# Kernel optimization log

Measured on AMD Instinct MI355X. Metric: run time of the kernel, lower is better.

## Reference

```python
import jax, jax.numpy as jnp
import numpy as np
import math

NUM_HEADS = 32
HEAD_SIZE = 128
NUM_KV_HEADS = 8
GROUP = NUM_HEADS // NUM_KV_HEADS  # num_queries_per_kv
NEG_FILL = -50000.0


def setup_inputs() -> dict:
    key = jax.random.key(0)
    k1, k2, k3 = jax.random.split(key, 3)
    B, S = 2, 2048
    query = jax.random.normal(k1, (B, S, NUM_HEADS * HEAD_SIZE), dtype=jnp.float32)
    kk = jax.random.normal(k2, (B, S, NUM_KV_HEADS * HEAD_SIZE), dtype=jnp.float32)
    vv = jax.random.normal(k3, (B, S, NUM_KV_HEADS * HEAD_SIZE), dtype=jnp.float32)
    return {"query": query, "key": kk, "value": vv}


def _gqa_attention(query, key, value):
    B, S, H = query.shape
    # [B, nh, S, d]
    q = query.reshape(B, S, NUM_HEADS, HEAD_SIZE).transpose(0, 2, 1, 3)
    # expand kv heads to nh via group broadcast (matches expand+reshape in torch)
    k = key.reshape(B, S, NUM_KV_HEADS, HEAD_SIZE)
    k = jnp.broadcast_to(k[:, :, :, None, :], (B, S, NUM_KV_HEADS, GROUP, HEAD_SIZE))
    k = k.reshape(B, S, NUM_HEADS, HEAD_SIZE).transpose(0, 2, 1, 3)
    v = value.reshape(B, S, NUM_KV_HEADS, HEAD_SIZE)
    v = jnp.broadcast_to(v[:, :, :, None, :], (B, S, NUM_KV_HEADS, GROUP, HEAD_SIZE))
    v = v.reshape(B, S, NUM_HEADS, HEAD_SIZE).transpose(0, 2, 1, 3)

    scale = 1.0 / math.sqrt(HEAD_SIZE)  # code uses sqrt(d_k), not self.scale
    scores = jnp.einsum('bhqd,bhkd->bhqk', q, k) * scale  # [B, nh, S, S]
    causal = jnp.tril(jnp.ones((S, S), dtype=bool))  # subsequent_mask
    scores = jnp.where(causal[None, None, :, :], scores, NEG_FILL)
    p_attn = jax.nn.softmax(scores, axis=-1)
    out = jnp.einsum('bhqk,bhkd->bhqd', p_attn, v)  # [B, nh, S, d]
    return out.transpose(0, 2, 1, 3).reshape(B, S, H)


def reference(query, key, value):
    return _gqa_attention(query, key, value)
```

## Files before the change

kernel.cpp:

```cpp
#include <hip/hip_runtime.h>
#include <hip/hip_bf16.h>


namespace {
constexpr int NH = 32;
constexpr int HD = 128;
constexpr int KVH = 8;
constexpr int SEQ = 2048;
constexpr int NB = 2;
constexpr int QSTRIDE = NH * HD;
constexpr int KSTRIDE = KVH * HD;
constexpr float SCALE = 0.08838834764831845f;
constexpr float SCALE2 = 0.12751744f;

typedef __attribute__((ext_vector_type(8))) short short8;
typedef __attribute__((ext_vector_type(8))) __bf16 bf16x8;
typedef __attribute__((ext_vector_type(4))) float f32x4;
typedef __attribute__((ext_vector_type(16))) float f32x16;
typedef __attribute__((ext_vector_type(2))) unsigned uint2v;
typedef __attribute__((ext_vector_type(4))) unsigned uint4v;

__device__ inline short cvt_bf16(float f) {
  unsigned u = __builtin_bit_cast(unsigned, f);
  unsigned r = (u + 0x7fffu + ((u >> 16) & 1u)) >> 16;
  return (short)r;
}

__device__ inline short8 cvt8(const float* p) {
  f32x4 a = *(const f32x4*)p;
  f32x4 b = *(const f32x4*)(p + 4);
  short8 r;
#pragma unroll
  for (int j = 0; j < 4; ++j) {
    r[j] = cvt_bf16(a[j]);
    r[j + 4] = cvt_bf16(b[j]);
  }
  return r;
}

__device__ inline short8 cvt8s(const float* p, float sc) {
  f32x4 a = *(const f32x4*)p;
  f32x4 b = *(const f32x4*)(p + 4);
  short8 r;
#pragma unroll
  for (int j = 0; j < 4; ++j) {
    r[j] = cvt_bf16(a[j] * sc);
    r[j + 4] = cvt_bf16(b[j] * sc);
  }
  return r;
}

__device__ inline bf16x8 asbf(short8 s) { return __builtin_bit_cast(bf16x8, s); }

__device__ inline unsigned cvt_pk_bf16(float lo, float hi) {
  unsigned r;
  asm("v_cvt_pk_bf16_f32 %0, %1, %2" : "=v"(r) : "v"(lo), "v"(hi));
  return r;
}

__device__ inline float fast_exp2(float x) {
#if __has_builtin(__builtin_amdgcn_exp2f)
  return __builtin_amdgcn_exp2f(x);
#else
  return __expf(x * 0.6931471805599453f);
#endif
}

__device__ inline void swap_halves(unsigned a, unsigned b, unsigned& lo,
                                   unsigned& hi, int half) {
#if __has_builtin(__builtin_amdgcn_permlane32_swap)
  (void)half;
  uint2v r = __builtin_amdgcn_permlane32_swap(a, b, false, false);
  lo = r[0];
  hi = r[1];
#else
  unsigned axf = (unsigned)__shfl_xor((int)a, 32);
  unsigned bxf = (unsigned)__shfl_xor((int)b, 32);
  lo = half ? bxf : a;
  hi = half ? b : axf;
#endif
}
}

__global__ __launch_bounds__(256) void convert_kv(const float* __restrict__ K,
                                                  const float* __restrict__ V,
                                                  short* __restrict__ Kbf,
                                                  short* __restrict__ Vtb) {
  __shared__ __align__(16) short t_sh[32 * 136];
  int bid = blockIdx.x;
  int tid = threadIdx.x;
  if (bid < 2048) {
    int flat = bid * 256 + tid;
    int c16 = flat & 15;
    int kvh = (flat >> 4) & 7;
    int s = (flat >> 7) & 2047;
    int b = flat >> 18;
    int dsrc = (c16 ^ (s & 7)) << 3;
    const float* src = K + ((size_t)(b * SEQ + s)) * KSTRIDE + kvh * HD + dsrc;
    short* dst = Kbf + ((size_t)(b * KVH + kvh) * SEQ + s) * HD + (c16 << 3);
    *(short8*)dst = cvt8(src);
    return;
  }
  bid -= 2048;
  int s0 = (bid & 63) * 32;
  int kvh = (bid >> 6) & 7;
  int b = bid >> 9;
  {
    int si = tid >> 3;
    int dseg = (tid & 7) * 16;
    const float* src = V + ((size_t)(b * SEQ + s0 + si)) * KSTRIDE + kvh * HD + dseg;
    short8 a0 = cvt8(src);
    short8 a1 = cvt8(src + 8);
    *(short8*)&t_sh[si * 136 + dseg] = a0;
    *(short8*)&t_sh[si * 136 + dseg + 8] = a1;
  }
  __syncthreads();
  {
    int d = tid >> 1;
    int sseg = (tid & 1) * 16;
    short8 o0, o1;
#pragma unroll
    for (int j = 0; j < 8; ++j) {
      o0[j] = t_sh[(sseg + j) * 136 + d];
      o1[j] = t_sh[(sseg + 8 + j) * 136 + d];
    }
    int m7 = d & 7;
    int cs0 = ((s0 & 63) >> 3) + (sseg >> 3);
    short* dstv = Vtb + (size_t)(b * KVH + kvh) * HD * SEQ +
                  (size_t)(s0 >> 6) * (HD * 64) + d * 64;
    *(short8*)(dstv + ((cs0 ^ m7) << 3)) = o0;
    *(short8*)(dstv + (((cs0 + 1) ^ m7) << 3)) = o1;
  }
}

__global__ __launch_bounds__(256, 2) void gqa_attn(
    const float* __restrict__ Q, const short* __restrict__ Kbf,
    const short* __restrict__ Vtb, float* __restrict__ O) {
  __shared__ __align__(16) short k_sh[2][64 * 128];
  __shared__ __align__(16) short v_sh[2][128 * 64];

  const int tid = threadIdx.x;
  const int wid = tid >> 6;
  const int lane = tid & 63;
  const int l31 = lane & 31;
  const int half = lane >> 5;
  const int vx = (((l31 & 7) ^ half) << 4);

  const int bid = blockIdx.x;
  const int qt = 15 - (bid >> 6);
  const int h = bid & 31;
  const int b = (bid >> 5) & 1;
  const int kvh = h >> 2;
  const int q0 = qt << 7;

  const int row_min = q0 + wid * 32;
  const int row_top = row_min + 31;
  const int qrow = row_min + l31;

  const float* qptr = Q + (size_t)(b * SEQ + qrow) * QSTRIDE + h * HD + half * 8;
  short8 qf[8];
#pragma unroll
  for (int st = 0; st < 8; ++st) qf[st] = cvt8s(qptr + st * 16, SCALE2);

  f32x16 acc[4];
#pragma unroll
  for (int t = 0; t < 4; ++t)
#pragma unroll
    for (int i = 0; i < 16; ++i) acc[t][i] = 0.f;
  float l_acc[2] = {0.f, 0.f};

  const char* kbase = (const char*)(Kbf + (size_t)(b * KVH + kvh) * SEQ * HD);
  const char* vbase = (const char*)(Vtb + (size_t)(b * KVH + kvh) * HD * SEQ);
  const int sgo = wid * 4096 + lane * 16;

  auto stage = [&](int bsel, int kb_) {
    const char* kg = kbase + (size_t)kb_ * 256 + sgo;
    const char* vg = vbase + (size_t)(kb_ >> 6) * 16384 + sgo;
    char* kl = (char*)&k_sh[bsel][0] + wid * 4096;
    char* vl = (char*)&v_sh[bsel][0] + wid * 4096;
#pragma unroll
    for (int i = 0; i < 4; ++i) {
      __builtin_amdgcn_global_load_lds((const void*)(kg + i * 1024),
                                       (void*)(kl + i * 1024), 16, 0, 0);
      __builtin_amdgcn_global_load_lds((const void*)(vg + i * 1024),
                                       (void*)(vl + i * 1024), 16, 0, 0);
    }
  };

  const int nT = 2 * qt + 2;
  stage(0, 0);

#pragma unroll 1
  for (int it = 0; it < nT; ++it) {
    const int kb = it << 6;
    const int cur = it & 1;
    __syncthreads();
    if (it + 1 < nT) stage(cur ^ 1, kb + 64);

    if (kb <= row_top) {
      const char* kB = (const char*)&k_sh[cur][0] + l31 * 256;
      const char* vB = (const char*)&v_sh[cur][0] + l31 * 128;

      f32x16 cS[2];
#pragma unroll
      for (int s = 0; s < 2; ++s)
#pragma unroll
        for (int i = 0; i < 16; ++i) cS[s][i] = 0.f;
#pragma unroll
      for (int st = 0; st < 8; ++st) {
        const int so = vx ^ (st << 5);
        bf16x8 qv = asbf(qf[st]);
        short8 k0 = *(const short8*)(kB + so);
        cS[0] = __builtin_amdgcn_mfma_f32_32x32x16_bf16(asbf(k0), qv, cS[0], 0, 0, 0);
        short8 k1 = *(const short8*)(kB + 8192 + so);
        cS[1] = __builtin_amdgcn_mfma_f32_32x32x16_bf16(asbf(k1), qv, cS[1], 0, 0, 0);
      }

      const bool diag = (kb + 63 > row_min);
      const int rel = qrow - kb - 4 * half;
#pragma unroll
      for (int s = 0; s < 2; ++s) {
        if (diag) {
#pragma unroll
          for (int r = 0; r < 16; ++r) {
            const int kc_ = (r & 3) + 8 * (r >> 2);
            float sc = cS[s][r];
            if (kc_ + s * 32 > rel) sc = -1e30f;
            float e = fast_exp2(sc);
            cS[s][r] = e;
            l_acc[s] += e;
          }
        } else {
#pragma unroll
          for (int r = 0; r < 16; ++r) {
            float e = fast_exp2(cS[s][r]);
            cS[s][r] = e;
            l_acc[s] += e;
          }
        }

        unsigned Ag[4], Bg[4];
#pragma unroll
        for (int g = 0; g < 4; ++g) {
          Ag[g] = cvt_pk_bf16(cS[s][4 * g], cS[s][4 * g + 1]);
          Bg[g] = cvt_pk_bf16(cS[s][4 * g + 2], cS[s][4 * g + 3]);
        }
#pragma unroll
        for (int kc = 0; kc < 2; ++kc) {
          unsigned a_lo, a_hi, b_lo, b_hi;
          swap_halves(Ag[2 * kc], Ag[2 * kc + 1], a_lo, a_hi, half);
          swap_halves(Bg[2 * kc], Bg[2 * kc + 1], b_lo, b_hi, half);
          uint4v wv;
          wv[0] = a_lo;
          wv[1] = b_lo;
          wv[2] = a_hi;
          wv[3] = b_hi;
          bf16x8 pa = __builtin_bit_cast(bf16x8, wv);
          const int vo = vx ^ ((s << 6) | (kc << 5));
#pragma unroll
          for (int t = 0; t < 4; ++t) {
            short8 vv = *(const short8*)(vB + t * 4096 + vo);
            acc[t] = __builtin_amdgcn_mfma_f32_32x32x16_bf16(pa, asbf(vv), acc[t], 0, 0, 0);
          }
        }
      }
    }
  }

  float l_part = l_acc[0] + l_acc[1];
  float lsum = l_part + __shfl_xor(l_part, 32);
  float invv = 1.f / lsum;
  float inv_i[16];
#pragma unroll
  for (int i = 0; i < 16; ++i)
    inv_i[i] = __shfl(invv, (i & 3) + 8 * (i >> 2) + 4 * half);
  float* ob = O + (size_t)(b * SEQ + row_min) * QSTRIDE + h * HD;
#pragma unroll
  for (int t = 0; t < 4; ++t)
#pragma unroll
    for (int i = 0; i < 16; ++i) {
      const int row = (i & 3) + 8 * (i >> 2) + 4 * half;
      ob[(size_t)row * QSTRIDE + t * 32 + l31] = acc[t][i] * inv_i[i];
    }
}

namespace {
constexpr int FKL = 136, FVL = 40, FPL = 40;
constexpr float NEGF = -50000.0f;
}
__global__ __launch_bounds__(256) void gqa_attn_f32(
    const float* __restrict__ Q, const float* __restrict__ K,
    const float* __restrict__ V, float* __restrict__ O) {
  __shared__ __align__(16) short k_sh[32 * FKL];
  __shared__ __align__(16) short v_sh[HD * FVL];
  __shared__ __align__(16) short p_sh[4 * 16 * FPL];
  const int tid = threadIdx.x, wid = tid >> 6, lane = tid & 63;
  const int col = lane & 15, quad = lane >> 4;
  const int bid = blockIdx.x;
  const int qt = bid & 31, h = (bid >> 5) & 31, b = bid >> 10;
  const int kvh = h >> 2, q0 = qt << 6;
  const int qrow = q0 + wid * 16 + col;
  const float* qptr = Q + (size_t)(b * SEQ + qrow) * QSTRIDE + h * HD + quad * 8;
  short8 qf[4];
#pragma unroll
  for (int c = 0; c < 4; ++c) qf[c] = cvt8(qptr + c * 32);
  f32x4 acc[8];
#pragma unroll
  for (int t = 0; t < 8; ++t) acc[t] = (f32x4){0.f, 0.f, 0.f, 0.f};
  float m_run[4] = {-1e30f, -1e30f, -1e30f, -1e30f};
  float l_run[4] = {0.f, 0.f, 0.f, 0.f};
  const float* kbase = K + (size_t)b * SEQ * KSTRIDE + kvh * HD;
  const float* vbase = V + (size_t)b * SEQ * KSTRIDE + kvh * HD;
  const int skey = tid & 31, sd = (tid >> 5) << 4;
  const int q_reg_row = q0 + wid * 16 + quad * 4;
  const int nT = (q0 >> 5) + 2;
  for (int it = 0; it < nT; ++it) {
    const int kb = it << 5;
    __syncthreads();
    {
      const float* ks = kbase + (size_t)(kb + skey) * KSTRIDE + sd;
      short8 k0 = cvt8(ks), k1 = cvt8(ks + 8);
      *(short8*)&k_sh[skey * FKL + sd] = k0;
      *(short8*)&k_sh[skey * FKL + sd + 8] = k1;
      const float* vs = vbase + (size_t)(kb + skey) * KSTRIDE + sd;
      short8 v0 = cvt8(vs), v1 = cvt8(vs + 8);
#pragma unroll
      for (int j = 0; j < 8; ++j) v_sh[(sd + j) * FVL + skey] = v0[j];
#pragma unroll
      for (int j = 0; j < 8; ++j) v_sh[(sd + 8 + j) * FVL + skey] = v1[j];
    }
    __syncthreads();
    f32x4 cL = {0.f, 0.f, 0.f, 0.f}, cR = {0.f, 0.f, 0.f, 0.f};
#pragma unroll
    for (int c = 0; c < 4; ++c) {
      short8 bL = *(const short8*)&k_sh[col * FKL + c * 32 + quad * 8];
      short8 bR = *(const short8*)&k_sh[(col + 16) * FKL + c * 32 + quad * 8];
      cL = __builtin_amdgcn_mfma_f32_16x16x32_bf16(asbf(qf[c]), asbf(bL), cL, 0, 0, 0);
      cR = __builtin_amdgcn_mfma_f32_16x16x32_bf16(asbf(qf[c]), asbf(bR), cR, 0, 0, 0);
    }
    float pL[4], pR[4], alpha[4];
#pragma unroll
    for (int r = 0; r < 4; ++r) {
      const int qr = q_reg_row + r;
      float sL = (kb + col <= qr) ? cL[r] * SCALE : NEGF;
      float sR = (kb + 16 + col <= qr) ? cR[r] * SCALE : NEGF;
      float mx = fmaxf(sL, sR);
      mx = fmaxf(mx, __shfl_xor(mx, 1));
      mx = fmaxf(mx, __shfl_xor(mx, 2));
      mx = fmaxf(mx, __shfl_xor(mx, 4));
      mx = fmaxf(mx, __shfl_xor(mx, 8));
      float nm = fmaxf(m_run[r], mx);
      alpha[r] = __expf(m_run[r] - nm);
      m_run[r] = nm;
      pL[r] = __expf(sL - nm);
      pR[r] = __expf(sR - nm);
      float ps = pL[r] + pR[r];
      ps += __shfl_xor(ps, 1);
      ps += __shfl_xor(ps, 2);
      ps += __shfl_xor(ps, 4);
      ps += __shfl_xor(ps, 8);
      l_run[r] = l_run[r] * alpha[r] + ps;
    }
#pragma unroll
    for (int t = 0; t < 8; ++t)
#pragma unroll
      for (int r = 0; r < 4; ++r) acc[t][r] *= alpha[r];
    short* pw = &p_sh[wid * 16 * FPL];
#pragma unroll
    for (int r = 0; r < 4; ++r) {
      pw[(quad * 4 + r) * FPL + col] = cvt_bf16(pL[r]);
      pw[(quad * 4 + r) * FPL + col + 16] = cvt_bf16(pR[r]);
    }
    __syncthreads();
    short8 pa = *(const short8*)&pw[col * FPL + quad * 8];
#pragma unroll
    for (int t = 0; t < 8; ++t) {
      short8 vb = *(const short8*)&v_sh[(t * 16 + col) * FVL + quad * 8];
      acc[t] = __builtin_amdgcn_mfma_f32_16x16x32_bf16(asbf(pa), asbf(vb), acc[t], 0, 0, 0);
    }
  }
  float inv[4];
#pragma unroll
  for (int r = 0; r < 4; ++r) inv[r] = 1.f / l_run[r];
  float* ob = O + (size_t)(b * SEQ + q_reg_row) * QSTRIDE + h * HD;
#pragma unroll
  for (int r = 0; r < 4; ++r)
#pragma unroll
    for (int t = 0; t < 8; ++t)
      ob[(size_t)r * QSTRIDE + t * 16 + col] = acc[t][r] * inv[r];
}

extern "C" void kernel_launch(void* const* d_in, const int* in_sizes, int n_in,
                              void* d_out, int out_size, void* d_ws, size_t ws_size,
                              hipStream_t stream) {
  const float* Q = (const float*)d_in[0];
  const float* K = (const float*)d_in[1];
  const float* V = (const float*)d_in[2];
  float* O = (float*)d_out;
  const size_t kv_elems = (size_t)NB * KVH * SEQ * HD;
  const size_t need = kv_elems * 2 * sizeof(short);
  if (ws_size >= need) {
    short* Kbf = (short*)d_ws;
    short* Vtb = Kbf + kv_elems;
    convert_kv<<<3072, 256, 0, stream>>>(K, V, Kbf, Vtb);
    gqa_attn<<<1024, 256, 0, stream>>>(Q, Kbf, Vtb, O);
  } else {
    gqa_attn_f32<<<2048, 256, 0, stream>>>(Q, K, V, O);
  }
}
```

Measured before the change: 208.9 us.

## Process two query heads per block to reuse staged K/V tiles

Each block now handles two query heads that share the same KV head, so every K/V tile staged into LDS and every K/V register fragment feeds two sets of MFMAs. The grid is halved to 512 blocks, and the query-tile order interleaves long and short causal tiles to balance the load. This halves LDS staging and K/V LDS reads per unit of work. In exchange it doubles the accumulator and Q-fragment register footprint, which may hurt occupancy under launch_bounds(256,2), and fewer blocks means less parallelism.

```diff
diff --git a/kernel.cpp b/kernel.cpp
--- a/kernel.cpp
+++ b/kernel.cpp
@@ -147,27 +147,32 @@
   const int vx = (((l31 & 7) ^ half) << 4);
 
   const int bid = blockIdx.x;
-  const int qt = 15 - (bid >> 6);
-  const int h = bid & 31;
-  const int b = (bid >> 5) & 1;
-  const int kvh = h >> 2;
+  const int g = bid >> 5;
+  const int qt = (bid < 256) ? (15 - g) : (g - 8);
+  const int idx = bid & 31;
+  const int hp = idx & 15;
+  const int b = idx >> 4;
+  const int h0 = hp * 2;
+  const int kvh = hp >> 1;
   const int q0 = qt << 7;
 
   const int row_min = q0 + wid * 32;
   const int row_top = row_min + 31;
   const int qrow = row_min + l31;
 
-  const float* qptr = Q + (size_t)(b * SEQ + qrow) * QSTRIDE + h * HD + half * 8;
-  short8 qf[8];
-#pragma unroll
-  for (int st = 0; st < 8; ++st) qf[st] = cvt8s(qptr + st * 16, SCALE2);
-
-  f32x16 acc[4];
+  const float* qp = Q + (size_t)(b * SEQ + qrow) * QSTRIDE + h0 * HD + half * 8;
+  short8 qa[8], qb[8];
+#pragma unroll
+  for (int st = 0; st < 8; ++st) qa[st] = cvt8s(qp + st * 16, SCALE2);
+#pragma unroll
+  for (int st = 0; st < 8; ++st) qb[st] = cvt8s(qp + HD + st * 16, SCALE2);
+
+  f32x16 acc0[4], acc1[4];
 #pragma unroll
   for (int t = 0; t < 4; ++t)
 #pragma unroll
-    for (int i = 0; i < 16; ++i) acc[t][i] = 0.f;
-  float l_acc[2] = {0.f, 0.f};
+    for (int i = 0; i < 16; ++i) { acc0[t][i] = 0.f; acc1[t][i] = 0.f; }
+  float la0 = 0.f, la1 = 0.f;
 
   const char* kbase = (const char*)(Kbf + (size_t)(b * KVH + kvh) * SEQ * HD);
   const char* vbase = (const char*)(Vtb + (size_t)(b * KVH + kvh) * HD * SEQ);
@@ -201,87 +206,109 @@
       const char* kB = (const char*)&k_sh[cur][0] + l31 * 256;
       const char* vB = (const char*)&v_sh[cur][0] + l31 * 128;
 
-      f32x16 cS[2];
-#pragma unroll
-      for (int s = 0; s < 2; ++s)
-#pragma unroll
-        for (int i = 0; i < 16; ++i) cS[s][i] = 0.f;
-#pragma unroll
-      for (int st = 0; st < 8; ++st) {
-        const int so = vx ^ (st << 5);
-        bf16x8 qv = asbf(qf[st]);
-        short8 k0 = *(const short8*)(kB + so);
-        cS[0] = __builtin_amdgcn_mfma_f32_32x32x16_bf16(asbf(k0), qv, cS[0], 0, 0, 0);
-        short8 k1 = *(const short8*)(kB + 8192 + so);
-        cS[1] = __builtin_amdgcn_mfma_f32_32x32x16_bf16(asbf(k1), qv, cS[1], 0, 0, 0);
-      }
-
       const bool diag = (kb + 63 > row_min);
       const int rel = qrow - kb - 4 * half;
+
 #pragma unroll
       for (int s = 0; s < 2; ++s) {
+        f32x16 c0, c1;
+#pragma unroll
+        for (int i = 0; i < 16; ++i) { c0[i] = 0.f; c1[i] = 0.f; }
+#pragma unroll
+        for (int st = 0; st < 8; ++st) {
+          const int so = vx ^ (st << 5);
+          short8 k0 = *(const short8*)(kB + s * 8192 + so);
+          bf16x8 kb16 = asbf(k0);
+          c0 = __builtin_amdgcn_mfma_f32_32x32x16_bf16(kb16, asbf(qa[st]), c0, 0, 0, 0);
+          c1 = __builtin_amdgcn_mfma_f32_32x32x16_bf16(kb16, asbf(qb[st]), c1, 0, 0, 0);
+        }
+
         if (diag) {
 #pragma unroll
           for (int r = 0; r < 16; ++r) {
-            const int kc_ = (r & 3) + 8 * (r >> 2);
-            float sc = cS[s][r];
-            if (kc_ + s * 32 > rel) sc = -1e30f;
-            float e = fast_exp2(sc);
-            cS[s][r] = e;
-            l_acc[s] += e;
+            const int kc_ = (r & 3) + 8 * (r >> 2) + s * 32;
+            const bool msk = kc_ > rel;
+            float s0v = msk ? -1e30f : c0[r];
+            float s1v = msk ? -1e30f : c1[r];
+            float e0 = fast_exp2(s0v);
+            float e1 = fast_exp2(s1v);
+            c0[r] = e0; la0 += e0;
+            c1[r] = e1; la1 += e1;
           }
         } else {
 #pragma unroll
           for (int r = 0; r < 16; ++r) {
-            float e = fast_exp2(cS[s][r]);
-            cS[s][r] = e;
-            l_acc[s] += e;
+            float e0 = fast_exp2(c0[r]);
+            float e1 = fast_exp2(c1[r]);
+            c0[r] = e0; la0 += e0;
+            c1[r] = e1; la1 += e1;
           }
         }
 
-        unsigned Ag[4], Bg[4];
-#pragma unroll
-        for (int g = 0; g < 4; ++g) {
-          Ag[g] = cvt_pk_bf16(cS[s][4 * g], cS[s][4 * g + 1]);
-          Bg[g] = cvt_pk_bf16(cS[s][4 * g + 2], cS[s][4 * g + 3]);
+        bf16x8 pa0[2], pa1[2];
+        {
+          unsigned Ag[4], Bg[4];
+#pragma unroll
+          for (int g2 = 0; g2 < 4; ++g2) {
+            Ag[g2] = cvt_pk_bf16(c0[4 * g2], c0[4 * g2 + 1]);
+            Bg[g2] = cvt_pk_bf16(c0[4 * g2 + 2], c0[4 * g2 + 3]);
+          }
+#pragma unroll
+          for (int kc = 0; kc < 2; ++kc) {
+            unsigned a_lo, a_hi, b_lo, b_hi;
+            swap_halves(Ag[2 * kc], Ag[2 * kc + 1], a_lo, a_hi, half);
+            swap_halves(Bg[2 * kc], Bg[2 * kc + 1], b_lo, b_hi, half);
+            uint4v wv;
+            wv[0] = a_lo; wv[1] = b_lo; wv[2] = a_hi; wv[3] = b_hi;
+            pa0[kc] = __builtin_bit_cast(bf16x8, wv);
+          }
+#pragma unroll
+          for (int g2 = 0; g2 < 4; ++g2) {
+            Ag[g2] = cvt_pk_bf16(c1[4 * g2], c1[4 * g2 + 1]);
+            Bg[g2] = cvt_pk_bf16(c1[4 * g2 + 2], c1[4 * g2 + 3]);
+          }
+#pragma unroll
+          for (int kc = 0; kc < 2; ++kc) {
+            unsigned a_lo, a_hi, b_lo, b_hi;
+            swap_halves(Ag[2 * kc], Ag[2 * kc + 1], a_lo, a_hi, half);
+            swap_halves(Bg[2 * kc], Bg[2 * kc + 1], b_lo, b_hi, half);
+            uint4v wv;
+            wv[0] = a_lo; wv[1] = b_lo; wv[2] = a_hi; wv[3] = b_hi;
+            pa1[kc] = __builtin_bit_cast(bf16x8, wv);
+          }
         }
+
 #pragma unroll
         for (int kc = 0; kc < 2; ++kc) {
-          unsigned a_lo, a_hi, b_lo, b_hi;
-          swap_halves(Ag[2 * kc], Ag[2 * kc + 1], a_lo, a_hi, half);
-          swap_halves(Bg[2 * kc], Bg[2 * kc + 1], b_lo, b_hi, half);
-          uint4v wv;
-          wv[0] = a_lo;
-          wv[1] = b_lo;
-          wv[2] = a_hi;
-          wv[3] = b_hi;
-          bf16x8 pa = __builtin_bit_cast(bf16x8, wv);
           const int vo = vx ^ ((s << 6) | (kc << 5));
 #pragma unroll
           for (int t = 0; t < 4; ++t) {
             short8 vv = *(const short8*)(vB + t * 4096 + vo);
-            acc[t] = __builtin_amdgcn_mfma_f32_32x32x16_bf16(pa, asbf(vv), acc[t], 0, 0, 0);
+            bf16x8 vb16 = asbf(vv);
+            acc0[t] = __builtin_amdgcn_mfma_f32_32x32x16_bf16(pa0[kc], vb16, acc0[t], 0, 0, 0);
+            acc1[t] = __builtin_amdgcn_mfma_f32_32x32x16_bf16(pa1[kc], vb16, acc1[t], 0, 0, 0);
           }
         }
       }
     }
   }
 
-  float l_part = l_acc[0] + l_acc[1];
-  float lsum = l_part + __shfl_xor(l_part, 32);
-  float invv = 1.f / lsum;
-  float inv_i[16];
-#pragma unroll
-  for (int i = 0; i < 16; ++i)
-    inv_i[i] = __shfl(invv, (i & 3) + 8 * (i >> 2) + 4 * half);
-  float* ob = O + (size_t)(b * SEQ + row_min) * QSTRIDE + h * HD;
-#pragma unroll
-  for (int t = 0; t < 4; ++t)
-#pragma unroll
-    for (int i = 0; i < 16; ++i) {
-      const int row = (i & 3) + 8 * (i >> 2) + 4 * half;
-      ob[(size_t)row * QSTRIDE + t * 32 + l31] = acc[t][i] * inv_i[i];
-    }
+  float ls0 = la0 + __shfl_xor(la0, 32);
+  float ls1 = la1 + __shfl_xor(la1, 32);
+  float iv0 = 1.f / ls0;
+  float iv1 = 1.f / ls1;
+  float* ob = O + (size_t)(b * SEQ + row_min) * QSTRIDE + h0 * HD;
+#pragma unroll
+  for (int i = 0; i < 16; ++i) {
+    const int row = (i & 3) + 8 * (i >> 2) + 4 * half;
+    const float v0 = __shfl(iv0, row & 31);
+    const float v1 = __shfl(iv1, row & 31);
+#pragma unroll
+    for (int t = 0; t < 4; ++t) {
+      ob[(size_t)row * QSTRIDE + t * 32 + l31] = acc0[t][i] * v0;
+      ob[(size_t)row * QSTRIDE + HD + t * 32 + l31] = acc1[t][i] * v1;
+    }
+  }
 }
 
 namespace {
@@ -403,7 +430,7 @@
     short* Kbf = (short*)d_ws;
     short* Vtb = Kbf + kv_elems;
     convert_kv<<<3072, 256, 0, stream>>>(K, V, Kbf, Vtb);
-    gqa_attn<<<1024, 256, 0, stream>>>(Q, Kbf, Vtb, O);
+    gqa_attn<<<512, 256, 0, stream>>>(Q, Kbf, Vtb, O);
   } else {
     gqa_attn_f32<<<2048, 256, 0, stream>>>(Q, K, V, O);
   }
```

Result: slower. 262.6 us (+25.7%).

## Compute softmax row sums with MFMA against ones and interleave QK per subtile

Applied to the files above, without the earlier changes.

Replaces the per-lane scalar accumulation of exponentials and the final shuffles with an extra MFMA that multiplies the bf16 probability tile by a ones matrix, producing row sums directly in the output layout. It also restructures the QK^T computation to run per 32-column subtile inside the softmax loop, reducing live score registers. The sums are now taken from bf16-rounded probabilities, consistent with what is fed to PV, at the cost of one extra MFMA per PV k-chunk and a 16-register accumulator.

```diff
diff --git a/kernel.cpp b/kernel.cpp
--- a/kernel.cpp
+++ b/kernel.cpp
@@ -162,12 +162,19 @@
 #pragma unroll
   for (int st = 0; st < 8; ++st) qf[st] = cvt8s(qptr + st * 16, SCALE2);
 
+  short8 ones_s;
+#pragma unroll
+  for (int j = 0; j < 8; ++j) ones_s[j] = (short)0x3F80;
+  const bf16x8 ONES = asbf(ones_s);
+
   f32x16 acc[4];
 #pragma unroll
   for (int t = 0; t < 4; ++t)
 #pragma unroll
     for (int i = 0; i < 16; ++i) acc[t][i] = 0.f;
-  float l_acc[2] = {0.f, 0.f};
+  f32x16 lacc;
+#pragma unroll
+  for (int i = 0; i < 16; ++i) lacc[i] = 0.f;
 
   const char* kbase = (const char*)(Kbf + (size_t)(b * KVH + kvh) * SEQ * HD);
   const char* vbase = (const char*)(Vtb + (size_t)(b * KVH + kvh) * HD * SEQ);
@@ -200,50 +207,39 @@
     if (kb <= row_top) {
       const char* kB = (const char*)&k_sh[cur][0] + l31 * 256;
       const char* vB = (const char*)&v_sh[cur][0] + l31 * 128;
-
-      f32x16 cS[2];
-#pragma unroll
-      for (int s = 0; s < 2; ++s)
-#pragma unroll
-        for (int i = 0; i < 16; ++i) cS[s][i] = 0.f;
-#pragma unroll
-      for (int st = 0; st < 8; ++st) {
-        const int so = vx ^ (st << 5);
-        bf16x8 qv = asbf(qf[st]);
-        short8 k0 = *(const short8*)(kB + so);
-        cS[0] = __builtin_amdgcn_mfma_f32_32x32x16_bf16(asbf(k0), qv, cS[0], 0, 0, 0);
-        short8 k1 = *(const short8*)(kB + 8192 + so);
-        cS[1] = __builtin_amdgcn_mfma_f32_32x32x16_bf16(asbf(k1), qv, cS[1], 0, 0, 0);
-      }
-
       const bool diag = (kb + 63 > row_min);
       const int rel = qrow - kb - 4 * half;
+
 #pragma unroll
       for (int s = 0; s < 2; ++s) {
+        f32x16 cS;
+#pragma unroll
+        for (int i = 0; i < 16; ++i) cS[i] = 0.f;
+#pragma unroll
+        for (int st = 0; st < 8; ++st) {
+          const int so = vx ^ (st << 5);
+          short8 k0 = *(const short8*)(kB + s * 8192 + so);
+          cS = __builtin_amdgcn_mfma_f32_32x32x16_bf16(asbf(k0), asbf(qf[st]), cS, 0, 0, 0);
+        }
+
         if (diag) {
 #pragma unroll
           for (int r = 0; r < 16; ++r) {
             const int kc_ = (r & 3) + 8 * (r >> 2);
-            float sc = cS[s][r];
+            float sc = cS[r];
             if (kc_ + s * 32 > rel) sc = -1e30f;
-            float e = fast_exp2(sc);
-            cS[s][r] = e;
-            l_acc[s] += e;
+            cS[r] = fast_exp2(sc);
           }
         } else {
 #pragma unroll
-          for (int r = 0; r < 16; ++r) {
-            float e = fast_exp2(cS[s][r]);
-            cS[s][r] = e;
-            l_acc[s] += e;
-          }
+          for (int r = 0; r < 16; ++r) cS[r] = fast_exp2(cS[r]);
         }
 
         unsigned Ag[4], Bg[4];
 #pragma unroll
-        for (int g = 0; g < 4; ++g) {
-          Ag[g] = cvt_pk_bf16(cS[s][4 * g], cS[s][4 * g + 1]);
-          Bg[g] = cvt_pk_bf16(cS[s][4 * g + 2], cS[s][4 * g + 3]);
+        for (int g2 = 0; g2 < 4; ++g2) {
+          Ag[g2] = cvt_pk_bf16(cS[4 * g2], cS[4 * g2 + 1]);
+          Bg[g2] = cvt_pk_bf16(cS[4 * g2 + 2], cS[4 * g2 + 3]);
         }
 #pragma unroll
         for (int kc = 0; kc < 2; ++kc) {
@@ -256,6 +252,7 @@
           wv[2] = a_hi;
           wv[3] = b_hi;
           bf16x8 pa = __builtin_bit_cast(bf16x8, wv);
+          lacc = __builtin_amdgcn_mfma_f32_32x32x16_bf16(pa, ONES, lacc, 0, 0, 0);
           const int vo = vx ^ ((s << 6) | (kc << 5));
 #pragma unroll
           for (int t = 0; t < 4; ++t) {
@@ -267,13 +264,9 @@
     }
   }
 
-  float l_part = l_acc[0] + l_acc[1];
-  float lsum = l_part + __shfl_xor(l_part, 32);
-  float invv = 1.f / lsum;
   float inv_i[16];
 #pragma unroll
-  for (int i = 0; i < 16; ++i)
-    inv_i[i] = __shfl(invv, (i & 3) + 8 * (i >> 2) + 4 * half);
+  for (int i = 0; i < 16; ++i) inv_i[i] = 1.f / lacc[i];
   float* ob = O + (size_t)(b * SEQ + row_min) * QSTRIDE + h * HD;
 #pragma unroll
   for (int t = 0; t < 4; ++t)
```

Measured after the change: 209.7 us. Within noise of the previous version (+0.4%).
